# Kernel tuning notes

Measured on AMD Instinct MI355X. Metric: run time of the kernel, lower is better.

Reference implementation:

```python
import math
import jax, jax.numpy as jnp
import numpy as np

B, L, D, H = 2, 2048, 1024, 16
HD = D // H
EPS = 1e-6
ROPE_BASE = 10000.0


def setup_inputs() -> dict:
    key = jax.random.key(0)
    ks = jax.random.split(key, 6)
    s = 0.02
    return {
        "z_H_previous": jax.random.normal(ks[0], (B, L, D), jnp.float32),
        "z_L_current": jax.random.normal(ks[1], (B, L, D), jnp.float32),
        "w_qkv": jax.random.normal(ks[2], (3 * D, D), jnp.float32) * s,
        "w_out": jax.random.normal(ks[3], (D, D), jnp.float32) * s,
        "w_ffn1": jax.random.normal(ks[4], (4 * D, D), jnp.float32) * s,
        "w_ffn2": jax.random.normal(ks[5], (D, 4 * D), jnp.float32) * s,
        "g_norm1": jnp.ones((D,), jnp.float32),
        "g_norm2": jnp.ones((D,), jnp.float32),
    }


def _rmsnorm(x, g):
    # mean of squares over last dim, rsqrt, scale
    ms = jnp.mean(x * x, axis=-1, keepdims=True)
    return x * jax.lax.rsqrt(ms + EPS) * g


def _rope(x):
    # x: [b, h, l, hd]; non-interleaved rotate-half RoPE
    l, d = x.shape[-2], x.shape[-1]
    half = d // 2
    inv_freq = 1.0 / (ROPE_BASE ** (jnp.arange(half, dtype=jnp.float32) / half))
    freqs = jnp.arange(l, dtype=jnp.float32)[:, None] * inv_freq[None, :]  # [l, half]
    cos, sin = jnp.cos(freqs), jnp.sin(freqs)
    x1, x2 = x[..., :half], x[..., half:]
    return jnp.concatenate([x1 * cos - x2 * sin, x2 * cos + x1 * sin], axis=-1)


def reference(z_H_previous, z_L_current, w_qkv, w_out, w_ffn1, w_ffn2, g_norm1, g_norm2):
    x = z_H_previous + z_L_current                       # [b, l, d]
    h = _rmsnorm(x, g_norm1)
    b, l, d = h.shape
    qkv = h @ w_qkv.T                                    # [b, l, 3d]
    qkv = qkv.reshape(b, l, 3, H, HD).transpose(2, 0, 3, 1, 4)  # [3, b, h, l, hd]
    q, k, v = qkv[0], qkv[1], qkv[2]
    q = _rope(q)
    k = _rope(k)
    scores = jnp.einsum("bhqd,bhkd->bhqk", q, k) / math.sqrt(HD)
    attn = jax.nn.softmax(scores, axis=-1)
    out = jnp.einsum("bhqk,bhkd->bhqd", attn, v)         # [b, h, l, hd]
    out = out.transpose(0, 2, 1, 3).reshape(b, l, d)
    x = x + out @ w_out.T
    h2 = _rmsnorm(x, g_norm2)
    ffn = jax.nn.silu(h2 @ w_ffn1.T) @ w_ffn2.T
    return x + ffn
```

## Files before the change

kernel.cpp:

```cpp
#include <hip/hip_runtime.h>

typedef __bf16 bf16;
typedef __bf16 bf16x2 __attribute__((ext_vector_type(2)));
typedef __bf16 bf16x8 __attribute__((ext_vector_type(8)));
typedef __bf16 bf16x4 __attribute__((ext_vector_type(4)));
typedef float  f32x4  __attribute__((ext_vector_type(4)));
typedef float  f32x16 __attribute__((ext_vector_type(16)));
typedef unsigned int uint;

static __device__ __forceinline__ void async_copy16(const void* g, void* l) {
  __builtin_amdgcn_global_load_lds((__attribute__((address_space(1))) void*)g,
                                   (__attribute__((address_space(3))) void*)l,
                                   16, 0, 0);
}

static __device__ __forceinline__ uint pkbf2(float a, float b) {
  union { bf16x2 v; uint u; } x;
  x.v[0] = (bf16)a; x.v[1] = (bf16)b;
  return x.u;
}

union U4 { uint u[4]; bf16x8 v; };

__global__ __launch_bounds__(256) void f2b_kernel(const float* __restrict__ in,
                                                  bf16* __restrict__ out, int n4) {
  int i = blockIdx.x * 256 + threadIdx.x;
  if (i < n4) {
    float4 v = ((const float4*)in)[i];
    bf16x4 o;
    o[0] = (bf16)v.x; o[1] = (bf16)v.y; o[2] = (bf16)v.z; o[3] = (bf16)v.w;
    ((bf16x4*)out)[i] = o;
  }
}

__global__ __launch_bounds__(256)
void add_rmsnorm_kernel(const float* __restrict__ a, const float* __restrict__ b,
                        const float* __restrict__ g, float* __restrict__ xout,
                        bf16* __restrict__ hout) {
  const int row = blockIdx.x;
  const int tid = threadIdx.x;
  const size_t base = (size_t)row * 1024 + tid * 4;
  float4 x = *(const float4*)(a + base);
  if (b) {
    float4 y = *(const float4*)(b + base);
    x.x += y.x; x.y += y.y; x.z += y.z; x.w += y.w;
  }
  float ss = x.x*x.x + x.y*x.y + x.z*x.z + x.w*x.w;
#pragma unroll
  for (int off = 32; off > 0; off >>= 1) ss += __shfl_xor(ss, off, 64);
  __shared__ float red[4];
  const int wave = tid >> 6, lane = tid & 63;
  if (lane == 0) red[wave] = ss;
  __syncthreads();
  const float total = red[0] + red[1] + red[2] + red[3];
  const float scale = rsqrtf(total * (1.0f / 1024.0f) + 1e-6f);
  if (xout) *(float4*)(xout + base) = x;
  float4 gv = *(const float4*)(g + tid * 4);
  bf16x4 h;
  h[0] = (bf16)(x.x * scale * gv.x);
  h[1] = (bf16)(x.y * scale * gv.y);
  h[2] = (bf16)(x.z * scale * gv.z);
  h[3] = (bf16)(x.w * scale * gv.w);
  *(bf16x4*)(hout + base) = h;
}

__global__ __launch_bounds__(256) void rope_kernel(bf16* __restrict__ qk) {
  int idx = blockIdx.x * 256 + threadIdx.x;
  const int hd = idx & 31; idx >>= 5;
  const int l  = idx & 2047; idx >>= 11;
  const int h  = idx & 15; idx >>= 4;
  const int b  = idx & 1;  idx >>= 1;
  bf16* p = qk + (size_t)idx * 4194304 + ((size_t)(b * 16 + h) * 2048 + l) * 64;
  const float inv = powf(10000.0f, -(float)hd * (1.0f / 32.0f));
  const float fr = (float)l * inv;
  float s, c; sincosf(fr, &s, &c);
  const float x1 = (float)p[hd], x2 = (float)p[hd + 32];
  p[hd]      = (bf16)(x1 * c - x2 * s);
  p[hd + 32] = (bf16)(x2 * c + x1 * s);
}

enum { EP_QKV = 0, EP_ADD_RESID = 1, EP_SILU = 2 };

template <int MODE>
__global__ __launch_bounds__(256)
void gemm_bt(const bf16* __restrict__ A, const bf16* __restrict__ W,
             const float* __restrict__ resid, float* __restrict__ outF,
             bf16* __restrict__ outB, bf16* __restrict__ outB2,
             int M, int N, int K) {
  __shared__ bf16 As[128 * 32];
  __shared__ bf16 Bs[128 * 32];
  const int tid  = threadIdx.x;
  const int wave = tid >> 6;
  const int lane = tid & 63;
  const int quad = lane >> 4;
  const int l16  = lane & 15;

  const int nb = N >> 7;
  const int bm = blockIdx.x / nb;
  const int bn = blockIdx.x - bm * nb;
  const int m0 = bm << 7, n0 = bn << 7;
  const int wm = (wave >> 1) << 6;
  const int wn = (wave & 1) << 6;

  const int srow = wave * 32 + (lane >> 2);
  const int scol = (((lane & 3) ^ ((lane >> 3) & 3)) * 8);
  const bf16* gA = A + (size_t)(m0 + srow) * K + scol;
  const bf16* gB = W + (size_t)(n0 + srow) * K + scol;
  bf16* lA0 = &As[(wave * 32) * 32];
  bf16* lA1 = &As[(wave * 32 + 16) * 32];
  bf16* lB0 = &Bs[(wave * 32) * 32];
  bf16* lB1 = &Bs[(wave * 32 + 16) * 32];

  const int sw = (l16 >> 1) & 3;
  f32x4 acc[4][4] = {};

  for (int k0 = 0; k0 < K; k0 += 32) {
    __syncthreads();
    async_copy16(gA, lA0);
    async_copy16(gA + (size_t)16 * K, lA1);
    async_copy16(gB, lB0);
    async_copy16(gB + (size_t)16 * K, lB1);
    gA += 32; gB += 32;
    __syncthreads();
    bf16x8 af[4], bfr[4];
#pragma unroll
    for (int i = 0; i < 4; i++)
      af[i] = *(const bf16x8*)&As[(wm + i * 16 + l16) * 32 + ((quad ^ sw) * 8)];
#pragma unroll
    for (int j = 0; j < 4; j++)
      bfr[j] = *(const bf16x8*)&Bs[(wn + j * 16 + l16) * 32 + ((quad ^ sw) * 8)];
#pragma unroll
    for (int i = 0; i < 4; i++)
#pragma unroll
      for (int j = 0; j < 4; j++)
        acc[i][j] = __builtin_amdgcn_mfma_f32_16x16x32_bf16(af[i], bfr[j], acc[i][j], 0, 0, 0);
  }

#pragma unroll
  for (int i = 0; i < 4; i++) {
    const int mbase = m0 + wm + i * 16 + quad * 4;
#pragma unroll
    for (int j = 0; j < 4; j++) {
      const int n = n0 + wn + j * 16 + l16;
      f32x4 v = acc[i][j];
#pragma unroll
      for (int r = 0; r < 4; r++) {
        const int m = mbase + r;
        const float val = v[r];
        if constexpr (MODE == EP_QKV) {
          const int bb = m >> 11, l = m & 2047;
          const int which = n >> 10, hh = (n >> 6) & 15, hd = n & 63;
          if (which == 2) {
            outB2[((size_t)(bb * 16 + hh) * 64 + hd) * 2048 + l] = (bf16)val;
          } else {
            const float sc = (which == 0) ? 0.1803368801111243f : 1.0f;
            outB[(((size_t)(which * 2 + bb) * 16 + hh) * 2048 + l) * 64 + hd] = (bf16)(val * sc);
          }
        } else if constexpr (MODE == EP_ADD_RESID) {
          outF[(size_t)m * N + n] = val + resid[(size_t)m * N + n];
        } else {
          outB[(size_t)m * N + n] = (bf16)(val / (1.0f + __expf(-val)));
        }
      }
    }
  }
}

__global__ __launch_bounds__(256)
void gemm_bt_splitk(const bf16* __restrict__ A, const bf16* __restrict__ W,
                    float* __restrict__ P, int M, int N, int Ktot) {
  __shared__ bf16 As[128 * 32];
  __shared__ bf16 Bs[128 * 32];
  const int tid  = threadIdx.x;
  const int wave = tid >> 6;
  const int lane = tid & 63;
  const int quad = lane >> 4;
  const int l16  = lane & 15;

  const int nb = N >> 7;
  const int tiles = (M >> 7) * nb;
  const int t = blockIdx.x % tiles;
  const int split = blockIdx.x / tiles;
  const int bm = t / nb, bn = t - bm * nb;
  const int m0 = bm << 7, n0 = bn << 7;
  const int wm = (wave >> 1) << 6;
  const int wn = (wave & 1) << 6;
  const int Kh = Ktot >> 1;
  const int koff = split * Kh;

  const int srow = wave * 32 + (lane >> 2);
  const int scol = (((lane & 3) ^ ((lane >> 3) & 3)) * 8);
  const bf16* gA = A + (size_t)(m0 + srow) * Ktot + koff + scol;
  const bf16* gB = W + (size_t)(n0 + srow) * Ktot + koff + scol;
  bf16* lA0 = &As[(wave * 32) * 32];
  bf16* lA1 = &As[(wave * 32 + 16) * 32];
  bf16* lB0 = &Bs[(wave * 32) * 32];
  bf16* lB1 = &Bs[(wave * 32 + 16) * 32];

  const int sw = (l16 >> 1) & 3;
  f32x4 acc[4][4] = {};

  for (int k0 = 0; k0 < Kh; k0 += 32) {
    __syncthreads();
    async_copy16(gA, lA0);
    async_copy16(gA + (size_t)16 * Ktot, lA1);
    async_copy16(gB, lB0);
    async_copy16(gB + (size_t)16 * Ktot, lB1);
    gA += 32; gB += 32;
    __syncthreads();
    bf16x8 af[4], bfr[4];
#pragma unroll
    for (int i = 0; i < 4; i++)
      af[i] = *(const bf16x8*)&As[(wm + i * 16 + l16) * 32 + ((quad ^ sw) * 8)];
#pragma unroll
    for (int j = 0; j < 4; j++)
      bfr[j] = *(const bf16x8*)&Bs[(wn + j * 16 + l16) * 32 + ((quad ^ sw) * 8)];
#pragma unroll
    for (int i = 0; i < 4; i++)
#pragma unroll
      for (int j = 0; j < 4; j++)
        acc[i][j] = __builtin_amdgcn_mfma_f32_16x16x32_bf16(af[i], bfr[j], acc[i][j], 0, 0, 0);
  }

  float* Pd = P + (size_t)split * M * N;
#pragma unroll
  for (int i = 0; i < 4; i++) {
    const int mbase = m0 + wm + i * 16 + quad * 4;
#pragma unroll
    for (int j = 0; j < 4; j++) {
      const int n = n0 + wn + j * 16 + l16;
#pragma unroll
      for (int r = 0; r < 4; r++)
        Pd[(size_t)(mbase + r) * N + n] = acc[i][j][r];
    }
  }
}

__global__ __launch_bounds__(256)
void splitk_combine(const float* __restrict__ P, const float* __restrict__ resid,
                    float* __restrict__ out, int total4) {
  int i = blockIdx.x * 256 + threadIdx.x;
  if (i < total4) {
    float4 a = ((const float4*)P)[i];
    float4 b = ((const float4*)(P + 4194304))[i];
    float4 r = ((const float4*)resid)[i];
    float4 o;
    o.x = a.x + b.x + r.x; o.y = a.y + b.y + r.y;
    o.z = a.z + b.z + r.z; o.w = a.w + b.w + r.w;
    ((float4*)out)[i] = o;
  }
}

__global__ __launch_bounds__(256)
void gemm64_bt(const bf16* __restrict__ A, const bf16* __restrict__ W,
               const float* __restrict__ resid, float* __restrict__ outF,
               int M, int N, int K) {
  __shared__ bf16 As[64 * 32];
  __shared__ bf16 Bs[128 * 32];
  const int tid = threadIdx.x, wave = tid >> 6, lane = tid & 63;
  const int quad = lane >> 4, l16 = lane & 15;
  const int nb = N >> 7;
  const int bm = blockIdx.x / nb, bn = blockIdx.x - bm * nb;
  const int m0 = bm << 6, n0 = bn << 7;
  const int wm = (wave >> 1) * 32, wn = (wave & 1) * 64;

  const int arow = wave * 16 + (lane >> 2);
  const int brow = wave * 32 + (lane >> 2);
  const int scol = (((lane & 3) ^ ((lane >> 3) & 3)) * 8);
  const bf16* gA = A + (size_t)(m0 + arow) * K + scol;
  const bf16* gB = W + (size_t)(n0 + brow) * K + scol;
  bf16* lA  = &As[(wave * 16) * 32];
  bf16* lB0 = &Bs[(wave * 32) * 32];
  bf16* lB1 = &Bs[(wave * 32 + 16) * 32];

  const int sw = (l16 >> 1) & 3;
  f32x4 acc[2][4] = {};
  for (int k0 = 0; k0 < K; k0 += 32) {
    __syncthreads();
    async_copy16(gA, lA);
    async_copy16(gB, lB0);
    async_copy16(gB + (size_t)16 * K, lB1);
    gA += 32; gB += 32;
    __syncthreads();
    bf16x8 af[2], bfr[4];
#pragma unroll
    for (int i = 0; i < 2; i++)
      af[i] = *(const bf16x8*)&As[(wm + i * 16 + l16) * 32 + ((quad ^ sw) * 8)];
#pragma unroll
    for (int j = 0; j < 4; j++)
      bfr[j] = *(const bf16x8*)&Bs[(wn + j * 16 + l16) * 32 + ((quad ^ sw) * 8)];
#pragma unroll
    for (int i = 0; i < 2; i++)
#pragma unroll
      for (int j = 0; j < 4; j++)
        acc[i][j] = __builtin_amdgcn_mfma_f32_16x16x32_bf16(af[i], bfr[j], acc[i][j], 0, 0, 0);
  }
#pragma unroll
  for (int i = 0; i < 2; i++) {
    const int mbase = m0 + wm + i * 16 + quad * 4;
#pragma unroll
    for (int j = 0; j < 4; j++) {
      const int n = n0 + wn + j * 16 + l16;
#pragma unroll
      for (int r = 0; r < 4; r++) {
        const int m = mbase + r;
        outF[(size_t)m * N + n] = acc[i][j][r] + resid[(size_t)m * N + n];
      }
    }
  }
}

__global__ __launch_bounds__(256, 4)
void attn_kernel(const bf16* __restrict__ qk, const bf16* __restrict__ vt,
                 bf16* __restrict__ Opart, float* __restrict__ Lpart) {
  const int qt    = blockIdx.x & 15;
  const int bh    = (blockIdx.x >> 4) & 31;
  const int split = blockIdx.x >> 9;
  const bf16* Qp = qk + (size_t)bh * 131072;
  const bf16* Kp = Qp + 4194304;
  const bf16* Vp = vt + (size_t)bh * 131072;

  const int tid = threadIdx.x, wave = tid >> 6, lane = tid & 63;
  const int hl = lane >> 5, l32 = lane & 31;
  const int qw = qt * 128 + wave * 32;

  __shared__ bf16 lds[9216];
  bf16* Ks = lds;
  bf16* Vs = lds + 4096;

  bf16x8 qf[4];
#pragma unroll
  for (int dk = 0; dk < 4; dk++)
    qf[dk] = *(const bf16x8*)&Qp[(size_t)(qw + l32) * 64 + dk * 16 + hl * 8];

  f32x16 o0 = {}, o1 = {};
  float l_i = 0.0f;

  const int rl = lane >> 3;
  const int cg = (lane & 7) ^ rl;

  const int kvbase = split * 512;
  for (int kv0 = kvbase; kv0 < kvbase + 512; kv0 += 64) {
    __syncthreads();
#pragma unroll
    for (int i = 0; i < 2; i++) {
      const int row = wave * 16 + i * 8;
      async_copy16(Kp + (size_t)(kv0 + row + rl) * 64 + cg * 8, &Ks[row * 64]);
      async_copy16(Vp + (size_t)(row + rl) * 2048 + kv0 + cg * 8, &Vs[row * 64]);
    }
    __syncthreads();

    f32x16 s0 = {}, s1 = {};
#pragma unroll
    for (int dk = 0; dk < 4; dk++) {
      const bf16x8 kf = *(const bf16x8*)&Ks[l32 * 64 + ((dk * 2 + hl) ^ (l32 & 7)) * 8];
      s0 = __builtin_amdgcn_mfma_f32_32x32x16_bf16(kf, qf[dk], s0, 0, 0, 0);
    }
#pragma unroll
    for (int dk = 0; dk < 4; dk++) {
      const bf16x8 kf = *(const bf16x8*)&Ks[(32 + l32) * 64 + ((dk * 2 + hl) ^ (l32 & 7)) * 8];
      s1 = __builtin_amdgcn_mfma_f32_32x32x16_bf16(kf, qf[dk], s1, 0, 0, 0);
    }

    U4 pf[4];
    float sum = 0.0f;
#pragma unroll
    for (int ks = 0; ks < 2; ks++) {
      const f32x16 sv = ks ? s1 : s0;
      uint d[8];
#pragma unroll
      for (int i = 0; i < 8; i++) {
        const float a = exp2f(sv[2 * i]);
        const float b = exp2f(sv[2 * i + 1]);
        sum += a + b;
        d[i] = pkbf2(a, b);
      }
      uint send0 = hl ? d[0] : d[2];
      uint send1 = hl ? d[1] : d[3];
      uint send2 = hl ? d[4] : d[6];
      uint send3 = hl ? d[5] : d[7];
      const uint r0 = __shfl_xor(send0, 32, 64);
      const uint r1 = __shfl_xor(send1, 32, 64);
      const uint r2 = __shfl_xor(send2, 32, 64);
      const uint r3 = __shfl_xor(send3, 32, 64);
      U4& f0 = pf[ks * 2];
      U4& f1 = pf[ks * 2 + 1];
      f0.u[0] = hl ? r0 : d[0];  f0.u[1] = hl ? r1 : d[1];
      f0.u[2] = hl ? d[2] : r0;  f0.u[3] = hl ? d[3] : r1;
      f1.u[0] = hl ? r2 : d[4];  f1.u[1] = hl ? r3 : d[5];
      f1.u[2] = hl ? d[6] : r2;  f1.u[3] = hl ? d[7] : r3;
    }
    l_i += sum + __shfl_xor(sum, 32, 64);

#pragma unroll
    for (int c16 = 0; c16 < 4; c16++) {
      const bf16x8 vf0 = *(const bf16x8*)&Vs[l32 * 64 + ((c16 * 2 + hl) ^ (l32 & 7)) * 8];
      const bf16x8 vf1 = *(const bf16x8*)&Vs[(32 + l32) * 64 + ((c16 * 2 + hl) ^ (l32 & 7)) * 8];
      o0 = __builtin_amdgcn_mfma_f32_32x32x16_bf16(vf0, pf[c16].v, o0, 0, 0, 0);
      o1 = __builtin_amdgcn_mfma_f32_32x32x16_bf16(vf1, pf[c16].v, o1, 0, 0, 0);
    }
  }

  Lpart[(size_t)(split * 32 + bh) * 2048 + qt * 128 + wave * 32 + l32] = l_i;

  __syncthreads();
  uint* L32 = (uint*)lds;
  const int qloc = wave * 32 + l32;
#pragma unroll
  for (int ds = 0; ds < 2; ds++) {
    const f32x16 ov = ds ? o1 : o0;
#pragma unroll
    for (int i = 0; i < 8; i++) {
      const int r = 2 * i;
      const int dd = ds * 32 + (r & 3) + 8 * (r >> 2) + 4 * hl;
      L32[qloc * 36 + (dd >> 1)] = pkbf2(ov[r], ov[r + 1]);
    }
  }
  __syncthreads();
#pragma unroll
  for (int p = 0; p < 4; p++) {
    const int qr = p * 32 + (tid >> 3), c = tid & 7;
    const uint4 v = *(const uint4*)&L32[qr * 36 + c * 4];
    *(uint4*)&Opart[(((size_t)(split * 32 + bh) * 2048) + qt * 128 + qr) * 64 + c * 8] = v;
  }
}

__global__ __launch_bounds__(256)
void attn_combine(const bf16* __restrict__ Opart, const float* __restrict__ Lpart,
                  bf16* __restrict__ out) {
  const int t = blockIdx.x * 256 + threadIdx.x;
  const int c = t & 7, qq = t >> 3;
  const int bh = qq >> 11, q = qq & 2047;
  const int b = bh >> 4, h = bh & 15;
  float acc[8] = {};
  float lsum = 0.0f;
#pragma unroll
  for (int s = 0; s < 4; s++) {
    const bf16x8 ov = *(const bf16x8*)&Opart[((size_t)(s * 32 + bh) * 2048 + q) * 64 + c * 8];
    lsum += Lpart[(size_t)(s * 32 + bh) * 2048 + q];
#pragma unroll
    for (int i = 0; i < 8; i++) acc[i] += (float)ov[i];
  }
  const float inv = 1.0f / lsum;
  bf16x8 o;
#pragma unroll
  for (int i = 0; i < 8; i++) o[i] = (bf16)(acc[i] * inv);
  *(bf16x8*)&out[((size_t)b * 2048 + q) * 1024 + h * 64 + c * 8] = o;
}

extern "C" void kernel_launch(void* const* d_in, const int* in_sizes, int n_in,
                              void* d_out, int out_size, void* d_ws, size_t ws_size,
                              hipStream_t stream) {
  (void)in_sizes; (void)n_in; (void)out_size; (void)ws_size;
  const float* zH    = (const float*)d_in[0];
  const float* zL    = (const float*)d_in[1];
  const float* w_qkv = (const float*)d_in[2];
  const float* w_out = (const float*)d_in[3];
  const float* w_f1  = (const float*)d_in[4];
  const float* w_f2  = (const float*)d_in[5];
  const float* g1    = (const float*)d_in[6];
  const float* g2    = (const float*)d_in[7];
  float* out = (float*)d_out;

  char* ws = (char*)d_ws;
  size_t off = 0;
  auto alloc = [&](size_t bytes) {
    void* p = ws + off;
    off += (bytes + 255) & ~(size_t)255;
    return p;
  };
  bf16*  bqkv  = (bf16*)alloc(3145728ull * 2);
  bf16*  bwout = (bf16*)alloc(1048576ull * 2);
  bf16*  bf1   = (bf16*)alloc(4194304ull * 2);
  bf16*  bf2   = (bf16*)alloc(4194304ull * 2);
  const size_t off_x = off;
  float* x     = (float*)alloc(4194304ull * 4);
  bf16*  hbuf  = (bf16*)alloc(4194304ull * 2);
  bf16*  qkb   = (bf16*)alloc(8388608ull * 2);
  bf16*  vtb   = (bf16*)alloc(4194304ull * 2);
  bf16*  attnb = (bf16*)alloc(4194304ull * 2);
  const size_t offU = off;
  float* x2    = (float*)alloc(4194304ull * 4);
  bf16*  h2    = (bf16*)alloc(4194304ull * 2);
  bf16*  act   = (bf16*)alloc(16777216ull * 2);
  bf16*  Opart = (bf16*)(ws + offU);
  float* Lpart = (float*)(ws + offU + 16777216ull * 2 + 256);
  float* Ppart = (float*)(ws + off_x);

  f2b_kernel<<<3072, 256, 0, stream>>>(w_qkv, bqkv, 3145728 / 4);
  f2b_kernel<<<1024, 256, 0, stream>>>(w_out, bwout, 1048576 / 4);
  f2b_kernel<<<4096, 256, 0, stream>>>(w_f1, bf1, 4194304 / 4);
  f2b_kernel<<<4096, 256, 0, stream>>>(w_f2, bf2, 4194304 / 4);

  add_rmsnorm_kernel<<<4096, 256, 0, stream>>>(zH, zL, g1, x, hbuf);

  gemm_bt<EP_QKV><<<768, 256, 0, stream>>>(hbuf, bqkv, nullptr, nullptr, qkb, vtb,
                                           4096, 3072, 1024);
  rope_kernel<<<16384, 256, 0, stream>>>(qkb);
  attn_kernel<<<2048, 256, 0, stream>>>(qkb, vtb, Opart, Lpart);
  attn_combine<<<2048, 256, 0, stream>>>(Opart, Lpart, attnb);

  gemm64_bt<<<512, 256, 0, stream>>>(attnb, bwout, x, x2, 4096, 1024, 1024);
  add_rmsnorm_kernel<<<4096, 256, 0, stream>>>(x2, nullptr, g2, nullptr, h2);
  gemm_bt<EP_SILU><<<1024, 256, 0, stream>>>(h2, bf1, nullptr, nullptr, act, nullptr,
                                             4096, 4096, 1024);
  gemm_bt_splitk<<<512, 256, 0, stream>>>(act, bf2, Ppart, 4096, 1024, 4096);
  splitk_combine<<<4096, 256, 0, stream>>>(Ppart, x2, out, 1048576);
}
```

Baseline: 420.1 us.

## Double GEMM K-tile to 64 with 8-way XOR swizzle and M-major block order

All three GEMM kernels now stage a K=64 slice per iteration instead of 32, which halves the number of barrier pairs per output tile and issues more async loads per sync. The LDS layout becomes 64-wide rows with an 8-group XOR swizzle to keep fragment reads conflict-free. Block indexing is also changed so consecutive blocks walk along M for a fixed N tile, which is meant to improve weight reuse in L2. The grid mapping now hardcodes the M-tile counts (32 or 64) instead of deriving them from M, and LDS use per block doubles, which may reduce occupancy.

```diff
diff --git a/kernel.cpp b/kernel.cpp
--- a/kernel.cpp
+++ b/kernel.cpp
@@ -87,53 +87,52 @@
              const float* __restrict__ resid, float* __restrict__ outF,
              bf16* __restrict__ outB, bf16* __restrict__ outB2,
              int M, int N, int K) {
-  __shared__ bf16 As[128 * 32];
-  __shared__ bf16 Bs[128 * 32];
+  __shared__ bf16 As[128 * 64];
+  __shared__ bf16 Bs[128 * 64];
   const int tid  = threadIdx.x;
   const int wave = tid >> 6;
   const int lane = tid & 63;
   const int quad = lane >> 4;
   const int l16  = lane & 15;
 
-  const int nb = N >> 7;
-  const int bm = blockIdx.x / nb;
-  const int bn = blockIdx.x - bm * nb;
+  const int bm = blockIdx.x & 31;
+  const int bn = blockIdx.x >> 5;
   const int m0 = bm << 7, n0 = bn << 7;
   const int wm = (wave >> 1) << 6;
   const int wn = (wave & 1) << 6;
 
-  const int srow = wave * 32 + (lane >> 2);
-  const int scol = (((lane & 3) ^ ((lane >> 3) & 3)) * 8);
-  const bf16* gA = A + (size_t)(m0 + srow) * K + scol;
-  const bf16* gB = W + (size_t)(n0 + srow) * K + scol;
-  bf16* lA0 = &As[(wave * 32) * 32];
-  bf16* lA1 = &As[(wave * 32 + 16) * 32];
-  bf16* lB0 = &Bs[(wave * 32) * 32];
-  bf16* lB1 = &Bs[(wave * 32 + 16) * 32];
-
-  const int sw = (l16 >> 1) & 3;
+  const int rl = lane >> 3;
+  const int cg = (lane & 7) ^ rl;
+  const bf16* gA = A + (size_t)(m0 + wave * 32 + rl) * K + cg * 8;
+  const bf16* gB = W + (size_t)(n0 + wave * 32 + rl) * K + cg * 8;
+
+  const int s8 = l16 & 7;
   f32x4 acc[4][4] = {};
 
-  for (int k0 = 0; k0 < K; k0 += 32) {
-    __syncthreads();
-    async_copy16(gA, lA0);
-    async_copy16(gA + (size_t)16 * K, lA1);
-    async_copy16(gB, lB0);
-    async_copy16(gB + (size_t)16 * K, lB1);
-    gA += 32; gB += 32;
-    __syncthreads();
-    bf16x8 af[4], bfr[4];
-#pragma unroll
-    for (int i = 0; i < 4; i++)
-      af[i] = *(const bf16x8*)&As[(wm + i * 16 + l16) * 32 + ((quad ^ sw) * 8)];
-#pragma unroll
-    for (int j = 0; j < 4; j++)
-      bfr[j] = *(const bf16x8*)&Bs[(wn + j * 16 + l16) * 32 + ((quad ^ sw) * 8)];
-#pragma unroll
-    for (int i = 0; i < 4; i++)
+  for (int k0 = 0; k0 < K; k0 += 64) {
+    __syncthreads();
+#pragma unroll
+    for (int i = 0; i < 4; i++) {
+      async_copy16(gA + (size_t)(i * 8) * K, &As[(wave * 32 + i * 8) * 64]);
+      async_copy16(gB + (size_t)(i * 8) * K, &Bs[(wave * 32 + i * 8) * 64]);
+    }
+    gA += 64; gB += 64;
+    __syncthreads();
+#pragma unroll
+    for (int kh = 0; kh < 2; kh++) {
+      bf16x8 af[4], bfr[4];
+#pragma unroll
+      for (int i = 0; i < 4; i++)
+        af[i] = *(const bf16x8*)&As[(wm + i * 16 + l16) * 64 + (((kh * 4 + quad) ^ s8) * 8)];
 #pragma unroll
       for (int j = 0; j < 4; j++)
-        acc[i][j] = __builtin_amdgcn_mfma_f32_16x16x32_bf16(af[i], bfr[j], acc[i][j], 0, 0, 0);
+        bfr[j] = *(const bf16x8*)&Bs[(wn + j * 16 + l16) * 64 + (((kh * 4 + quad) ^ s8) * 8)];
+#pragma unroll
+      for (int i = 0; i < 4; i++)
+#pragma unroll
+        for (int j = 0; j < 4; j++)
+          acc[i][j] = __builtin_amdgcn_mfma_f32_16x16x32_bf16(af[i], bfr[j], acc[i][j], 0, 0, 0);
+    }
   }
 
 #pragma unroll
@@ -169,57 +168,56 @@
 __global__ __launch_bounds__(256)
 void gemm_bt_splitk(const bf16* __restrict__ A, const bf16* __restrict__ W,
                     float* __restrict__ P, int M, int N, int Ktot) {
-  __shared__ bf16 As[128 * 32];
-  __shared__ bf16 Bs[128 * 32];
+  __shared__ bf16 As[128 * 64];
+  __shared__ bf16 Bs[128 * 64];
   const int tid  = threadIdx.x;
   const int wave = tid >> 6;
   const int lane = tid & 63;
   const int quad = lane >> 4;
   const int l16  = lane & 15;
 
-  const int nb = N >> 7;
-  const int tiles = (M >> 7) * nb;
-  const int t = blockIdx.x % tiles;
-  const int split = blockIdx.x / tiles;
-  const int bm = t / nb, bn = t - bm * nb;
+  const int r6 = blockIdx.x & 63;
+  const int bn = blockIdx.x >> 6;
+  const int bm = r6 >> 1;
+  const int split = r6 & 1;
   const int m0 = bm << 7, n0 = bn << 7;
   const int wm = (wave >> 1) << 6;
   const int wn = (wave & 1) << 6;
   const int Kh = Ktot >> 1;
   const int koff = split * Kh;
 
-  const int srow = wave * 32 + (lane >> 2);
-  const int scol = (((lane & 3) ^ ((lane >> 3) & 3)) * 8);
-  const bf16* gA = A + (size_t)(m0 + srow) * Ktot + koff + scol;
-  const bf16* gB = W + (size_t)(n0 + srow) * Ktot + koff + scol;
-  bf16* lA0 = &As[(wave * 32) * 32];
-  bf16* lA1 = &As[(wave * 32 + 16) * 32];
-  bf16* lB0 = &Bs[(wave * 32) * 32];
-  bf16* lB1 = &Bs[(wave * 32 + 16) * 32];
-
-  const int sw = (l16 >> 1) & 3;
+  const int rl = lane >> 3;
+  const int cg = (lane & 7) ^ rl;
+  const bf16* gA = A + (size_t)(m0 + wave * 32 + rl) * Ktot + koff + cg * 8;
+  const bf16* gB = W + (size_t)(n0 + wave * 32 + rl) * Ktot + koff + cg * 8;
+
+  const int s8 = l16 & 7;
   f32x4 acc[4][4] = {};
 
-  for (int k0 = 0; k0 < Kh; k0 += 32) {
-    __syncthreads();
-    async_copy16(gA, lA0);
-    async_copy16(gA + (size_t)16 * Ktot, lA1);
-    async_copy16(gB, lB0);
-    async_copy16(gB + (size_t)16 * Ktot, lB1);
-    gA += 32; gB += 32;
-    __syncthreads();
-    bf16x8 af[4], bfr[4];
-#pragma unroll
-    for (int i = 0; i < 4; i++)
-      af[i] = *(const bf16x8*)&As[(wm + i * 16 + l16) * 32 + ((quad ^ sw) * 8)];
-#pragma unroll
-    for (int j = 0; j < 4; j++)
-      bfr[j] = *(const bf16x8*)&Bs[(wn + j * 16 + l16) * 32 + ((quad ^ sw) * 8)];
-#pragma unroll
-    for (int i = 0; i < 4; i++)
+  for (int k0 = 0; k0 < Kh; k0 += 64) {
+    __syncthreads();
+#pragma unroll
+    for (int i = 0; i < 4; i++) {
+      async_copy16(gA + (size_t)(i * 8) * Ktot, &As[(wave * 32 + i * 8) * 64]);
+      async_copy16(gB + (size_t)(i * 8) * Ktot, &Bs[(wave * 32 + i * 8) * 64]);
+    }
+    gA += 64; gB += 64;
+    __syncthreads();
+#pragma unroll
+    for (int kh = 0; kh < 2; kh++) {
+      bf16x8 af[4], bfr[4];
+#pragma unroll
+      for (int i = 0; i < 4; i++)
+        af[i] = *(const bf16x8*)&As[(wm + i * 16 + l16) * 64 + (((kh * 4 + quad) ^ s8) * 8)];
 #pragma unroll
       for (int j = 0; j < 4; j++)
-        acc[i][j] = __builtin_amdgcn_mfma_f32_16x16x32_bf16(af[i], bfr[j], acc[i][j], 0, 0, 0);
+        bfr[j] = *(const bf16x8*)&Bs[(wn + j * 16 + l16) * 64 + (((kh * 4 + quad) ^ s8) * 8)];
+#pragma unroll
+      for (int i = 0; i < 4; i++)
+#pragma unroll
+        for (int j = 0; j < 4; j++)
+          acc[i][j] = __builtin_amdgcn_mfma_f32_16x16x32_bf16(af[i], bfr[j], acc[i][j], 0, 0, 0);
+    }
   }
 
   float* Pd = P + (size_t)split * M * N;
@@ -255,45 +253,47 @@
 void gemm64_bt(const bf16* __restrict__ A, const bf16* __restrict__ W,
                const float* __restrict__ resid, float* __restrict__ outF,
                int M, int N, int K) {
-  __shared__ bf16 As[64 * 32];
-  __shared__ bf16 Bs[128 * 32];
+  __shared__ bf16 As[64 * 64];
+  __shared__ bf16 Bs[128 * 64];
   const int tid = threadIdx.x, wave = tid >> 6, lane = tid & 63;
   const int quad = lane >> 4, l16 = lane & 15;
-  const int nb = N >> 7;
-  const int bm = blockIdx.x / nb, bn = blockIdx.x - bm * nb;
+  const int bm = blockIdx.x & 63;
+  const int bn = blockIdx.x >> 6;
   const int m0 = bm << 6, n0 = bn << 7;
   const int wm = (wave >> 1) * 32, wn = (wave & 1) * 64;
 
-  const int arow = wave * 16 + (lane >> 2);
-  const int brow = wave * 32 + (lane >> 2);
-  const int scol = (((lane & 3) ^ ((lane >> 3) & 3)) * 8);
-  const bf16* gA = A + (size_t)(m0 + arow) * K + scol;
-  const bf16* gB = W + (size_t)(n0 + brow) * K + scol;
-  bf16* lA  = &As[(wave * 16) * 32];
-  bf16* lB0 = &Bs[(wave * 32) * 32];
-  bf16* lB1 = &Bs[(wave * 32 + 16) * 32];
-
-  const int sw = (l16 >> 1) & 3;
+  const int rl = lane >> 3;
+  const int cg = (lane & 7) ^ rl;
+  const bf16* gA = A + (size_t)(m0 + wave * 16 + rl) * K + cg * 8;
+  const bf16* gB = W + (size_t)(n0 + wave * 32 + rl) * K + cg * 8;
+
+  const int s8 = l16 & 7;
   f32x4 acc[2][4] = {};
-  for (int k0 = 0; k0 < K; k0 += 32) {
-    __syncthreads();
-    async_copy16(gA, lA);
-    async_copy16(gB, lB0);
-    async_copy16(gB + (size_t)16 * K, lB1);
-    gA += 32; gB += 32;
-    __syncthreads();
-    bf16x8 af[2], bfr[4];
+  for (int k0 = 0; k0 < K; k0 += 64) {
+    __syncthreads();
 #pragma unroll
     for (int i = 0; i < 2; i++)
-      af[i] = *(const bf16x8*)&As[(wm + i * 16 + l16) * 32 + ((quad ^ sw) * 8)];
-#pragma unroll
-    for (int j = 0; j < 4; j++)
-      bfr[j] = *(const bf16x8*)&Bs[(wn + j * 16 + l16) * 32 + ((quad ^ sw) * 8)];
-#pragma unroll
-    for (int i = 0; i < 2; i++)
+      async_copy16(gA + (size_t)(i * 8) * K, &As[(wave * 16 + i * 8) * 64]);
+#pragma unroll
+    for (int i = 0; i < 4; i++)
+      async_copy16(gB + (size_t)(i * 8) * K, &Bs[(wave * 32 + i * 8) * 64]);
+    gA += 64; gB += 64;
+    __syncthreads();
+#pragma unroll
+    for (int kh = 0; kh < 2; kh++) {
+      bf16x8 af[2], bfr[4];
+#pragma unroll
+      for (int i = 0; i < 2; i++)
+        af[i] = *(const bf16x8*)&As[(wm + i * 16 + l16) * 64 + (((kh * 4 + quad) ^ s8) * 8)];
 #pragma unroll
       for (int j = 0; j < 4; j++)
-        acc[i][j] = __builtin_amdgcn_mfma_f32_16x16x32_bf16(af[i], bfr[j], acc[i][j], 0, 0, 0);
+        bfr[j] = *(const bf16x8*)&Bs[(wn + j * 16 + l16) * 64 + (((kh * 4 + quad) ^ s8) * 8)];
+#pragma unroll
+      for (int i = 0; i < 2; i++)
+#pragma unroll
+        for (int j = 0; j < 4; j++)
+          acc[i][j] = __builtin_amdgcn_mfma_f32_16x16x32_bf16(af[i], bfr[j], acc[i][j], 0, 0, 0);
+    }
   }
 #pragma unroll
   for (int i = 0; i < 2; i++) {
```

After: 380.0 us. -9.6%, faster.
